# Kernel optimization log

Hardware: AMD Instinct MI355X
Metric: run time of the kernel (lower is better)

## Reference

```python
import jax, jax.numpy as jnp
import numpy as np

SINKHORN_ALPHA = 20.0
WEIGHT_LOSS_ECR = 100.0
OT_MAX_ITER = 100
STOP_THR = 0.005
EPS = 1e-16


def setup_inputs() -> dict:
    key = jax.random.key(0)
    # cost matrix: [num_topics, vocab]
    M = jax.random.uniform(key, (512, 65536), dtype=jnp.float32)
    return {"M": M}


def reference(M) -> jnp.ndarray:
    n, m = M.shape
    a = jnp.full((n, 1), 1.0 / n, dtype=M.dtype)   # row marginal
    b = jnp.full((m, 1), 1.0 / m, dtype=M.dtype)   # col marginal
    u0 = jnp.full((n, 1), 1.0 / n, dtype=M.dtype)
    K = jnp.exp(-M * SINKHORN_ALPHA)               # [n, m]

    def cond_fn(carry):
        u, v, err, cpt = carry
        return (err > STOP_THR) & (cpt < OT_MAX_ITER)

    def body_fn(carry):
        u, v, err, cpt = carry
        v = b / (K.T @ u + EPS)                    # [m, 1]
        u = a / (K @ v + EPS)                      # [n, 1]
        cpt = cpt + 1
        # convergence check every 50 iters (cpt % 50 == 1), matching torch loop
        err = jax.lax.cond(
            cpt % 50 == 1,
            lambda: jnp.sum(jnp.abs(v * (K.T @ u) - b)).astype(err.dtype),
            lambda: err,
        )
        return (u, v, err, cpt)

    init = (u0, jnp.zeros((m, 1), dtype=M.dtype), jnp.asarray(1.0, M.dtype), jnp.asarray(0, jnp.int32))
    u, v, _, _ = jax.lax.while_loop(cond_fn, body_fn, init)

    transp = u * (K * v.T)                         # [n, m] transport plan
    loss_ECR = jnp.sum(transp * M) * WEIGHT_LOSS_ECR
    return loss_ECR
```

## Files before the change

### kernel.cpp

```cpp
#include <hip/hip_runtime.h>

#define NROW 512
#define NCOL 65536

static __device__ __forceinline__ float wave_sum(float x) {
  #pragma unroll
  for (int off = 32; off; off >>= 1) x += __shfl_down(x, off, 64);
  return x;
}

static __device__ __forceinline__ void gbar(int* cnt, int* phase) {
  __syncthreads();
  if (threadIdx.x == 0) {
    int ph = atomicAdd(phase, 0);
    __threadfence();
    if (atomicAdd(cnt, 1) == (int)gridDim.x - 1) {
      atomicExch(cnt, 0);
      __threadfence();
      atomicAdd(phase, 1);
    } else {
      while (atomicAdd(phase, 0) == ph) { __builtin_amdgcn_s_sleep(8); }
    }
    __threadfence();
  }
  __syncthreads();
}

__global__ __launch_bounds__(512)
void k1_colsum(const float* __restrict__ M, float* __restrict__ v,
               float* __restrict__ eA, int* __restrict__ bar) {
  const int tid = threadIdx.x, bid = blockIdx.x;
  const int chunk = tid & 31;
  const int part  = tid >> 5;
  const int col0  = (bid << 7) + (chunk << 2);
  const int r0    = part << 5;
  const float am = 1.0f / NROW, bm = 1.0f / NCOL, EPSV = 1e-16f;

  __shared__ float sCol[16 * 128];

  if (bid == 0 && tid < 8) eA[tid] = 0.f;
  if (bid == 0 && tid < 2) bar[tid] = 0;

  const float* Mp = M + (size_t)r0 * NCOL + col0;
  float4 cs = {0.f, 0.f, 0.f, 0.f};
  #pragma unroll 8
  for (int rr = 0; rr < 32; ++rr) {
    float4 m = *(const float4*)(Mp + (size_t)rr * NCOL);
    cs.x += __expf(-20.f * m.x);
    cs.y += __expf(-20.f * m.y);
    cs.z += __expf(-20.f * m.z);
    cs.w += __expf(-20.f * m.w);
  }
  *(float4*)(sCol + part * 128 + (chunk << 2)) = cs;
  __syncthreads();
  if (tid < 128) {
    float t = 0.f;
    #pragma unroll
    for (int p = 0; p < 16; ++p) t += sCol[p * 128 + tid];
    v[(bid << 7) + tid] = bm / (t * am + EPSV);
  }
}

__global__ __launch_bounds__(512)
void k2_rowdot(const float* __restrict__ M, const float* __restrict__ v,
               float* __restrict__ u) {
  const int tid = threadIdx.x, row = blockIdx.x;
  const float am = 1.0f / NROW, EPSV = 1e-16f;
  const float4* M4 = (const float4*)M + (size_t)row * (NCOL / 4);
  const float4* V4 = (const float4*)v;
  __shared__ float sRed[8];

  float acc = 0.f;
  #pragma unroll 8
  for (int it = 0; it < NCOL / 4 / 512; ++it) {
    const int c = (it << 9) + tid;
    float4 m = M4[c];
    float4 vv = V4[c];
    acc += __expf(-20.f * m.x) * vv.x + __expf(-20.f * m.y) * vv.y
         + __expf(-20.f * m.z) * vv.z + __expf(-20.f * m.w) * vv.w;
  }
  acc = wave_sum(acc);
  if ((tid & 63) == 0) sRed[tid >> 6] = acc;
  __syncthreads();
  if (tid == 0) {
    float s = 0.f;
    #pragma unroll
    for (int w = 0; w < 8; ++w) s += sRed[w];
    u[row] = am / (s + EPSV);
  }
}

__global__ __launch_bounds__(512)
void k3_colsum_u(const float* __restrict__ M, const float* __restrict__ v,
                 const float* __restrict__ u, float* __restrict__ tArr,
                 float* __restrict__ eA, float* __restrict__ out,
                 int* __restrict__ done) {
  const int tid = threadIdx.x, bid = blockIdx.x;
  const int chunk = tid & 31;
  const int part  = tid >> 5;
  const int col0  = (bid << 7) + (chunk << 2);
  const int r0    = part << 5;
  const float bm = 1.0f / NCOL;

  __shared__ float sU[NROW];
  __shared__ float sCol[16 * 128];
  __shared__ float sRed[8];

  sU[tid] = u[tid];
  __syncthreads();

  const float4 vv = *(const float4*)(v + col0);
  const float* Mp = M + (size_t)r0 * NCOL + col0;
  float4 cs = {0.f, 0.f, 0.f, 0.f};
  float lacc = 0.f;
  #pragma unroll 8
  for (int rr = 0; rr < 32; ++rr) {
    float4 m = *(const float4*)(Mp + (size_t)rr * NCOL);
    float e0 = __expf(-20.f * m.x), e1 = __expf(-20.f * m.y);
    float e2 = __expf(-20.f * m.z), e3 = __expf(-20.f * m.w);
    float us = sU[r0 + rr];
    cs.x = fmaf(e0, us, cs.x);
    cs.y = fmaf(e1, us, cs.y);
    cs.z = fmaf(e2, us, cs.z);
    cs.w = fmaf(e3, us, cs.w);
    lacc += us * (e0 * m.x * vv.x + e1 * m.y * vv.y
                + e2 * m.z * vv.z + e3 * m.w * vv.w);
  }
  *(float4*)(sCol + part * 128 + (chunk << 2)) = cs;
  lacc = wave_sum(lacc);
  if ((tid & 63) == 0) sRed[tid >> 6] = lacc;
  __syncthreads();

  float lblk = 0.f;
  if (tid == 0) {
    #pragma unroll
    for (int w = 0; w < 8; ++w) lblk += sRed[w];
  }
  float pe = 0.f;
  if (tid < 128) {
    float t = 0.f;
    #pragma unroll
    for (int p = 0; p < 16; ++p) t += sCol[p * 128 + tid];
    tArr[(bid << 7) + tid] = t;
    pe = fabsf(v[(bid << 7) + tid] * t - bm);
  }
  pe = wave_sum(pe);
  __syncthreads();
  if ((tid & 63) == 0) sRed[tid >> 6] = pe;
  __syncthreads();
  if (tid == 0) {
    float es = 0.f;
    #pragma unroll
    for (int w = 0; w < 8; ++w) es += sRed[w];
    atomicAdd(&eA[0], es);
    atomicAdd(&eA[2], lblk);
    __threadfence();
    int old = atomicAdd((int*)(eA + 4), 1);
    if (old == (int)gridDim.x - 1) {
      __threadfence();
      float err = atomicAdd(&eA[0], 0.f);
      float ls  = atomicAdd(&eA[2], 0.f);
      if (err <= 0.005f) { out[0] = 100.f * ls; done[0] = 1; }
      else               { out[0] = 0.f;        done[0] = 0; }
    }
  }
}

__global__ __launch_bounds__(1024)
void k5_fallback(const float* __restrict__ M, float* __restrict__ out,
                 float* __restrict__ v, float* __restrict__ u,
                 const float* __restrict__ tArr, float* __restrict__ eA,
                 const int* __restrict__ done, int* __restrict__ bar) {
  if (done[0]) return;
  const int tid = threadIdx.x, bid = blockIdx.x;
  const float am = 1.0f / NROW, bm = 1.0f / NCOL, EPSV = 1e-16f;
  int* cnt = bar;
  int* phs = bar + 1;

  __shared__ float sU[NROW];
  __shared__ float sCol[16 * 256];
  __shared__ float sRedA[16], sRedB[16];
  __shared__ float sErr;

  const int chunk = tid & 63;
  const int part  = tid >> 6;
  const int col0  = (bid << 8) + (chunk << 2);
  const int r0    = part << 5;
  const int row0  = bid << 1;

  float tt = (tid < 256) ? tArr[(bid << 8) + tid] : 0.f;

  int cpt = 1;
  while (true) {
    if (tid < 256) v[(bid << 8) + tid] = bm / (tt + EPSV);
    gbar(cnt, phs);
    cpt++;

    {
      const float4* M40 = (const float4*)M + (size_t)row0 * (NCOL / 4);
      const float4* M41 = (const float4*)M + (size_t)(row0 + 1) * (NCOL / 4);
      const float4* V4  = (const float4*)v;
      float ra = 0.f, rb = 0.f;
      #pragma unroll 4
      for (int it = 0; it < NCOL / 4 / 1024; ++it) {
        const int c = (it << 10) + tid;
        float4 vv = V4[c];
        float4 m0 = M40[c], m1 = M41[c];
        ra += __expf(-20.f * m0.x) * vv.x + __expf(-20.f * m0.y) * vv.y
            + __expf(-20.f * m0.z) * vv.z + __expf(-20.f * m0.w) * vv.w;
        rb += __expf(-20.f * m1.x) * vv.x + __expf(-20.f * m1.y) * vv.y
            + __expf(-20.f * m1.z) * vv.z + __expf(-20.f * m1.w) * vv.w;
      }
      ra = wave_sum(ra); rb = wave_sum(rb);
      if ((tid & 63) == 0) { sRedA[tid >> 6] = ra; sRedB[tid >> 6] = rb; }
      __syncthreads();
      if (tid < 2) {
        const float* sr = (tid == 0) ? sRedA : sRedB;
        float s = 0.f;
        #pragma unroll
        for (int w = 0; w < 16; ++w) s += sr[w];
        u[row0 + tid] = am / (s + EPSV);
      }
    }
    gbar(cnt, phs);
    if (cpt >= 100) break;

    if (tid < NROW) sU[tid] = u[tid];
    __syncthreads();
    float4 cs = {0.f, 0.f, 0.f, 0.f};
    #pragma unroll 4
    for (int r = r0; r < r0 + 32; ++r) {
      float4 m = *(const float4*)(M + (size_t)r * NCOL + col0);
      float us = sU[r];
      cs.x = fmaf(__expf(-20.f * m.x), us, cs.x);
      cs.y = fmaf(__expf(-20.f * m.y), us, cs.y);
      cs.z = fmaf(__expf(-20.f * m.z), us, cs.z);
      cs.w = fmaf(__expf(-20.f * m.w), us, cs.w);
    }
    *(float4*)(sCol + part * 256 + (chunk << 2)) = cs;
    __syncthreads();
    if (tid < 256) {
      tt = 0.f;
      #pragma unroll
      for (int p = 0; p < 16; ++p) tt += sCol[p * 256 + tid];
    }

    if (cpt == 51) {
      float pe = (tid < 256) ? fabsf(v[(bid << 8) + tid] * tt - bm) : 0.f;
      pe = wave_sum(pe);
      __syncthreads();
      if ((tid & 63) == 0) sRedA[tid >> 6] = pe;
      __syncthreads();
      if (tid == 0) {
        float s = 0.f;
        #pragma unroll
        for (int w = 0; w < 16; ++w) s += sRedA[w];
        atomicAdd(&eA[1], s);
      }
      gbar(cnt, phs);
      if (tid == 0) sErr = atomicAdd(&eA[1], 0.f);
      __syncthreads();
      if (sErr <= 0.005f) break;
    }
  }

  __syncthreads();
  if (tid < NROW) sU[tid] = u[tid];
  __syncthreads();
  {
    const float4 vv = *(const float4*)(v + col0);
    float lacc = 0.f;
    #pragma unroll 4
    for (int r = r0; r < r0 + 32; ++r) {
      float4 m = *(const float4*)(M + (size_t)r * NCOL + col0);
      float us = sU[r];
      lacc += us * (__expf(-20.f * m.x) * m.x * vv.x
                  + __expf(-20.f * m.y) * m.y * vv.y
                  + __expf(-20.f * m.z) * m.z * vv.z
                  + __expf(-20.f * m.w) * m.w * vv.w);
    }
    lacc = wave_sum(lacc);
    if ((tid & 63) == 0) sRedA[tid >> 6] = lacc;
    __syncthreads();
    if (tid == 0) {
      float s = 0.f;
      #pragma unroll
      for (int w = 0; w < 16; ++w) s += sRedA[w];
      atomicAdd(out, 100.f * s);
    }
  }
}

extern "C" void kernel_launch(void* const* d_in, const int* in_sizes, int n_in,
                              void* d_out, int out_size, void* d_ws, size_t ws_size,
                              hipStream_t stream) {
  const float* M = (const float*)d_in[0];
  float* out = (float*)d_out;

  const size_t offV = 0;
  const size_t offT = offV + (size_t)NCOL * sizeof(float);
  const size_t offU = offT + (size_t)NCOL * sizeof(float);
  const size_t offE = offU + 4096;
  const size_t offD = offE + 256;
  const size_t offB = offD + 256;
  const size_t need = offB + 256;
  if (ws_size < need) return;

  char* ws = (char*)d_ws;
  float* v    = (float*)(ws + offV);
  float* tArr = (float*)(ws + offT);
  float* u    = (float*)(ws + offU);
  float* eA   = (float*)(ws + offE);
  int*   done = (int*)(ws + offD);
  int*   bar  = (int*)(ws + offB);

  k1_colsum  <<<dim3(512), dim3(512), 0, stream>>>(M, v, eA, bar);
  k2_rowdot  <<<dim3(512), dim3(512), 0, stream>>>(M, v, u);
  k3_colsum_u<<<dim3(512), dim3(512), 0, stream>>>(M, v, u, tArr, eA, out, done);
  k5_fallback<<<dim3(256), dim3(1024), 0, stream>>>(M, out, v, u, tArr, eA,
                                                    done, bar);
}
```

Measured before the change: 252.6 us.

## Split column-sum kernels into two row bands with separate finalize kernels

The column-sum passes (initial v and the u-weighted column sums with loss accumulation) now run on 1024 blocks, each covering half the rows, and write partial sums to a new workspace buffer. Small follow-up kernels combine the two partials to produce v, or the column totals and the error check. The row-dot kernel moves to 1024-thread blocks. The aim is more parallelism and better latency hiding on the memory-bound passes over M, at the cost of two extra kernel launches and extra partial-buffer traffic.

```diff
diff --git a/kernel.cpp b/kernel.cpp
--- a/kernel.cpp
+++ b/kernel.cpp
@@ -27,14 +27,14 @@
 }
 
 __global__ __launch_bounds__(512)
-void k1_colsum(const float* __restrict__ M, float* __restrict__ v,
-               float* __restrict__ eA, int* __restrict__ bar) {
+void k1a_colsum(const float* __restrict__ M, float* __restrict__ tPart,
+                float* __restrict__ eA, int* __restrict__ bar) {
   const int tid = threadIdx.x, bid = blockIdx.x;
+  const int colblk = bid & 511, band = bid >> 9;
   const int chunk = tid & 31;
   const int part  = tid >> 5;
-  const int col0  = (bid << 7) + (chunk << 2);
-  const int r0    = part << 5;
-  const float am = 1.0f / NROW, bm = 1.0f / NCOL, EPSV = 1e-16f;
+  const int col0  = (colblk << 7) + (chunk << 2);
+  const int r0    = (band << 8) + (part << 4);
 
   __shared__ float sCol[16 * 128];
 
@@ -44,7 +44,7 @@
   const float* Mp = M + (size_t)r0 * NCOL + col0;
   float4 cs = {0.f, 0.f, 0.f, 0.f};
   #pragma unroll 8
-  for (int rr = 0; rr < 32; ++rr) {
+  for (int rr = 0; rr < 16; ++rr) {
     float4 m = *(const float4*)(Mp + (size_t)rr * NCOL);
     cs.x += __expf(-20.f * m.x);
     cs.y += __expf(-20.f * m.y);
@@ -57,23 +57,37 @@
     float t = 0.f;
     #pragma unroll
     for (int p = 0; p < 16; ++p) t += sCol[p * 128 + tid];
-    v[(bid << 7) + tid] = bm / (t * am + EPSV);
-  }
-}
-
-__global__ __launch_bounds__(512)
+    tPart[(size_t)band * NCOL + (colblk << 7) + tid] = t;
+  }
+}
+
+__global__ __launch_bounds__(256)
+void k1b_v1(const float* __restrict__ tPart, float* __restrict__ v) {
+  const int gid = blockIdx.x * 256 + threadIdx.x;
+  const int col0 = gid << 2;
+  const float am = 1.0f / NROW, bm = 1.0f / NCOL, EPSV = 1e-16f;
+  float4 p0 = *(const float4*)(tPart + col0);
+  float4 p1 = *(const float4*)(tPart + NCOL + col0);
+  float4 vv = {bm / ((p0.x + p1.x) * am + EPSV),
+               bm / ((p0.y + p1.y) * am + EPSV),
+               bm / ((p0.z + p1.z) * am + EPSV),
+               bm / ((p0.w + p1.w) * am + EPSV)};
+  *(float4*)(v + col0) = vv;
+}
+
+__global__ __launch_bounds__(1024)
 void k2_rowdot(const float* __restrict__ M, const float* __restrict__ v,
                float* __restrict__ u) {
   const int tid = threadIdx.x, row = blockIdx.x;
   const float am = 1.0f / NROW, EPSV = 1e-16f;
   const float4* M4 = (const float4*)M + (size_t)row * (NCOL / 4);
   const float4* V4 = (const float4*)v;
-  __shared__ float sRed[8];
+  __shared__ float sRed[16];
 
   float acc = 0.f;
-  #pragma unroll 8
-  for (int it = 0; it < NCOL / 4 / 512; ++it) {
-    const int c = (it << 9) + tid;
+  #pragma unroll 4
+  for (int it = 0; it < NCOL / 4 / 1024; ++it) {
+    const int c = (it << 10) + tid;
     float4 m = M4[c];
     float4 vv = V4[c];
     acc += __expf(-20.f * m.x) * vv.x + __expf(-20.f * m.y) * vv.y
@@ -85,40 +99,39 @@
   if (tid == 0) {
     float s = 0.f;
     #pragma unroll
-    for (int w = 0; w < 8; ++w) s += sRed[w];
+    for (int w = 0; w < 16; ++w) s += sRed[w];
     u[row] = am / (s + EPSV);
   }
 }
 
 __global__ __launch_bounds__(512)
-void k3_colsum_u(const float* __restrict__ M, const float* __restrict__ v,
-                 const float* __restrict__ u, float* __restrict__ tArr,
-                 float* __restrict__ eA, float* __restrict__ out,
-                 int* __restrict__ done) {
+void k3a_colsum_u(const float* __restrict__ M, const float* __restrict__ v,
+                  const float* __restrict__ u, float* __restrict__ tPart,
+                  float* __restrict__ eA) {
   const int tid = threadIdx.x, bid = blockIdx.x;
+  const int colblk = bid & 511, band = bid >> 9;
   const int chunk = tid & 31;
   const int part  = tid >> 5;
-  const int col0  = (bid << 7) + (chunk << 2);
-  const int r0    = part << 5;
-  const float bm = 1.0f / NCOL;
-
-  __shared__ float sU[NROW];
+  const int col0  = (colblk << 7) + (chunk << 2);
+  const int r0l   = part << 4;
+
+  __shared__ float sU[256];
   __shared__ float sCol[16 * 128];
   __shared__ float sRed[8];
 
-  sU[tid] = u[tid];
+  if (tid < 256) sU[tid] = u[(band << 8) + tid];
   __syncthreads();
 
   const float4 vv = *(const float4*)(v + col0);
-  const float* Mp = M + (size_t)r0 * NCOL + col0;
+  const float* Mp = M + (size_t)((band << 8) + r0l) * NCOL + col0;
   float4 cs = {0.f, 0.f, 0.f, 0.f};
   float lacc = 0.f;
   #pragma unroll 8
-  for (int rr = 0; rr < 32; ++rr) {
+  for (int rr = 0; rr < 16; ++rr) {
     float4 m = *(const float4*)(Mp + (size_t)rr * NCOL);
     float e0 = __expf(-20.f * m.x), e1 = __expf(-20.f * m.y);
     float e2 = __expf(-20.f * m.z), e3 = __expf(-20.f * m.w);
-    float us = sU[r0 + rr];
+    float us = sU[r0l + rr];
     cs.x = fmaf(e0, us, cs.x);
     cs.y = fmaf(e1, us, cs.y);
     cs.z = fmaf(e2, us, cs.z);
@@ -130,30 +143,39 @@
   lacc = wave_sum(lacc);
   if ((tid & 63) == 0) sRed[tid >> 6] = lacc;
   __syncthreads();
-
-  float lblk = 0.f;
-  if (tid == 0) {
-    #pragma unroll
-    for (int w = 0; w < 8; ++w) lblk += sRed[w];
-  }
-  float pe = 0.f;
   if (tid < 128) {
     float t = 0.f;
     #pragma unroll
     for (int p = 0; p < 16; ++p) t += sCol[p * 128 + tid];
-    tArr[(bid << 7) + tid] = t;
-    pe = fabsf(v[(bid << 7) + tid] * t - bm);
-  }
+    tPart[(size_t)band * NCOL + (colblk << 7) + tid] = t;
+  }
+  if (tid == 0)
+    atomicAdd(&eA[2], sRed[0] + sRed[1] + sRed[2] + sRed[3]
+                    + sRed[4] + sRed[5] + sRed[6] + sRed[7]);
+}
+
+__global__ __launch_bounds__(256)
+void k3b_err(const float* __restrict__ tPart, const float* __restrict__ v,
+             float* __restrict__ tArr, float* __restrict__ eA,
+             float* __restrict__ out, int* __restrict__ done) {
+  const int tid = threadIdx.x;
+  const int gid = blockIdx.x * 256 + tid;
+  const int col0 = gid << 2;
+  const float bm = 1.0f / NCOL;
+  __shared__ float sRed[4];
+
+  float4 p0 = *(const float4*)(tPart + col0);
+  float4 p1 = *(const float4*)(tPart + NCOL + col0);
+  float4 t = {p0.x + p1.x, p0.y + p1.y, p0.z + p1.z, p0.w + p1.w};
+  *(float4*)(tArr + col0) = t;
+  float4 vv = *(const float4*)(v + col0);
+  float pe = fabsf(vv.x * t.x - bm) + fabsf(vv.y * t.y - bm)
+           + fabsf(vv.z * t.z - bm) + fabsf(vv.w * t.w - bm);
   pe = wave_sum(pe);
-  __syncthreads();
   if ((tid & 63) == 0) sRed[tid >> 6] = pe;
   __syncthreads();
   if (tid == 0) {
-    float es = 0.f;
-    #pragma unroll
-    for (int w = 0; w < 8; ++w) es += sRed[w];
-    atomicAdd(&eA[0], es);
-    atomicAdd(&eA[2], lblk);
+    atomicAdd(&eA[0], sRed[0] + sRed[1] + sRed[2] + sRed[3]);
     __threadfence();
     int old = atomicAdd((int*)(eA + 4), 1);
     if (old == (int)gridDim.x - 1) {
@@ -303,20 +325,24 @@
   const size_t offE = offU + 4096;
   const size_t offD = offE + 256;
   const size_t offB = offD + 256;
-  const size_t need = offB + 256;
+  const size_t offP = offB + 256;
+  const size_t need = offP + 2 * (size_t)NCOL * sizeof(float);
   if (ws_size < need) return;
 
   char* ws = (char*)d_ws;
-  float* v    = (float*)(ws + offV);
-  float* tArr = (float*)(ws + offT);
-  float* u    = (float*)(ws + offU);
-  float* eA   = (float*)(ws + offE);
-  int*   done = (int*)(ws + offD);
-  int*   bar  = (int*)(ws + offB);
-
-  k1_colsum  <<<dim3(512), dim3(512), 0, stream>>>(M, v, eA, bar);
-  k2_rowdot  <<<dim3(512), dim3(512), 0, stream>>>(M, v, u);
-  k3_colsum_u<<<dim3(512), dim3(512), 0, stream>>>(M, v, u, tArr, eA, out, done);
-  k5_fallback<<<dim3(256), dim3(1024), 0, stream>>>(M, out, v, u, tArr, eA,
-                                                    done, bar);
-}
+  float* v     = (float*)(ws + offV);
+  float* tArr  = (float*)(ws + offT);
+  float* u     = (float*)(ws + offU);
+  float* eA    = (float*)(ws + offE);
+  int*   done  = (int*)(ws + offD);
+  int*   bar   = (int*)(ws + offB);
+  float* tPart = (float*)(ws + offP);
+
+  k1a_colsum  <<<dim3(1024), dim3(512),  0, stream>>>(M, tPart, eA, bar);
+  k1b_v1      <<<dim3(64),   dim3(256),  0, stream>>>(tPart, v);
+  k2_rowdot   <<<dim3(512),  dim3(1024), 0, stream>>>(M, v, u);
+  k3a_colsum_u<<<dim3(1024), dim3(512),  0, stream>>>(M, v, u, tPart, eA);
+  k3b_err     <<<dim3(64),   dim3(256),  0, stream>>>(tPart, v, tArr, eA, out, done);
+  k5_fallback <<<dim3(256),  dim3(1024), 0, stream>>>(M, out, v, u, tArr, eA,
+                                                      done, bar);
+}
```

Result: faster. 243.3 us (-3.7%).
